# Performance work log

Hardware: AMD Instinct MI355X
Metric: run time of the kernel (lower is better)

## Reference

```python
import jax, jax.numpy as jnp
import numpy as np

N, E, F_NODE, F_EDGE = 100000, 400000, 64, 16
HID, HEADS, L, G, FP = 128, 4, 4, 1024, 2048
DH = HID // HEADS
T, K = 5, 32
EPS = 1e-5
NEG_SLOPE = 0.2


def _gat(x, src, dst, ea, Wl, bl, Wr, br, We, att, bias):
    """GATv2Conv (PyG semantics, eval mode): x_l=lin_l(x_src), x_r=lin_r(x_dst),
    e = att . leaky_relu(x_l[src] + x_r[dst] + lin_edge(edge_attr)),
    alpha = segment-softmax over dst, out = scatter-sum(alpha * x_l[src]) + bias."""
    n = x.shape[0]
    xl = (x @ Wl + bl).reshape(n, HEADS, DH)
    xr = (x @ Wr + br).reshape(n, HEADS, DH)
    ee = (ea @ We).reshape(-1, HEADS, DH)
    e = jax.nn.leaky_relu(xl[src] + xr[dst] + ee, NEG_SLOPE)  # [E,H,D]
    score = jnp.einsum('ehd,hd->eh', e, att)                   # [E,H]
    m = jax.ops.segment_max(score, dst, num_segments=n)        # stable softmax
    p = jnp.exp(score - m[dst])
    denom = jax.ops.segment_sum(p, dst, num_segments=n)
    alpha = p / (denom[dst] + 1e-16)
    out = jax.ops.segment_sum(alpha[:, :, None] * xl[src], dst, num_segments=n)
    return out.reshape(n, HID) + bias


def _bn_elu(h, g, b):
    # BatchNorm over the node dimension (training-mode batch stats) + ELU
    mu = h.mean(0)
    var = h.var(0)
    return jax.nn.elu((h - mu) / jnp.sqrt(var + EPS) * g + b)


def setup_inputs() -> dict:
    key = jax.random.key(0)
    ks = jax.random.split(key, 16)
    s_in = 1.0 / np.sqrt(F_NODE)
    s_h = 1.0 / np.sqrt(HID)
    s_e = 1.0 / np.sqrt(F_EDGE)
    Lh = L - 1
    return dict(
        x=jax.random.normal(ks[0], (N, F_NODE), jnp.float32),
        edge_index=jax.random.randint(ks[1], (2, E), 0, N),
        edge_attr=jax.random.normal(ks[2], (E, F_EDGE), jnp.float32),
        batch=jnp.sort(jax.random.randint(ks[3], (N,), 0, G)),
        morgan_fp=(jax.random.uniform(ks[4], (G, FP)) < 0.1).astype(jnp.float32),
        fp_idx=jnp.arange(T * K).reshape(T, K),
        Wl0=jax.random.normal(ks[5], (F_NODE, HID)) * s_in,
        bl0=jnp.zeros((HID,)),
        Wr0=jax.random.normal(ks[6], (F_NODE, HID)) * s_in,
        br0=jnp.zeros((HID,)),
        We0=jax.random.normal(ks[7], (F_EDGE, HID)) * s_e,
        att0=jax.random.normal(ks[8], (HEADS, DH)) * s_h,
        bias0=jnp.zeros((HID,)),
        g0=jnp.ones((HID,)),
        b0=jnp.zeros((HID,)),
        Wl=jax.random.normal(ks[9], (Lh, HID, HID)) * s_h,
        bl=jnp.zeros((Lh, HID)),
        Wr=jax.random.normal(ks[10], (Lh, HID, HID)) * s_h,
        br=jnp.zeros((Lh, HID)),
        We=jax.random.normal(ks[11], (Lh, F_EDGE, HID)) * s_e,
        att=jax.random.normal(ks[12], (Lh, HEADS, DH)) * s_h,
        biasc=jnp.zeros((Lh, HID)),
        g=jnp.ones((Lh, HID)),
        b=jnp.zeros((Lh, HID)),
        tw1=jax.random.normal(ks[13], (T, HID + K, HID)) / np.sqrt(HID + K),
        tb1=jnp.zeros((T, HID)),
        tw2=jax.random.normal(ks[14], (T, HID, 1)) * s_h,
        tb2=jnp.zeros((T, 1)),
    )


def reference(x, edge_index, edge_attr, batch, morgan_fp, fp_idx,
              Wl0, bl0, Wr0, br0, We0, att0, bias0, g0, b0,
              Wl, bl, Wr, br, We, att, biasc, g, b,
              tw1, tb1, tw2, tb2):
    src, dst = edge_index[0], edge_index[1]
    h = _bn_elu(_gat(x, src, dst, edge_attr, Wl0, bl0, Wr0, br0, We0, att0, bias0), g0, b0)
    for i in range(L - 1):  # residual stacked GATv2 layers
        h = _bn_elu(_gat(h, src, dst, edge_attr, Wl[i], bl[i], Wr[i], br[i],
                         We[i], att[i], biasc[i]), g[i], b[i]) + h
    counts = jax.ops.segment_sum(jnp.ones((h.shape[0],), h.dtype), batch, num_segments=G)
    emb = jax.ops.segment_sum(h, batch, num_segments=G) / jnp.maximum(counts, 1.0)[:, None]
    outs = []
    for t in range(T):  # per-task heads on [graph_emb ; selected fp bits]
        fused = jnp.concatenate([emb, morgan_fp[:, fp_idx[t]]], axis=1)
        hm = jax.nn.relu(fused @ tw1[t] + tb1[t])
        outs.append(hm @ tw2[t] + tb2[t])
    return jnp.concatenate(outs, axis=1)  # [G, T]
```

## Files before the change

### kernel.cpp

```cpp
#include <hip/hip_runtime.h>
#include <hip/hip_bf16.h>

#define N_NODES 100000
#define N_EDGES 400000
#define F_NODE_ 64
#define F_EDGE_ 16
#define HID_ 128
#define N_GRAPH 1024
#define N_TASK 5

typedef unsigned short u16;
typedef __attribute__((ext_vector_type(8))) short frag8;
typedef __attribute__((ext_vector_type(4))) float f32x4;
typedef __attribute__((ext_vector_type(2))) float f32x2;

__device__ __forceinline__ float bu2f(u16 v){ return __uint_as_float(((unsigned)v) << 16); }
__device__ __forceinline__ float2 bp2f(unsigned u){
  return make_float2(__uint_as_float(u << 16), __uint_as_float(u & 0xFFFF0000u));
}
__device__ __forceinline__ f32x2 bp2v(unsigned u){
  f32x2 r; r.x = __uint_as_float(u << 16); r.y = __uint_as_float(u & 0xFFFF0000u); return r;
}
__device__ __forceinline__ u16 f2bu(float f){
  __hip_bfloat16 h = __float2bfloat16(f);
  return *(u16*)&h;
}
__device__ __forceinline__ unsigned packbf(float a, float b){
  return (unsigned)f2bu(a) | ((unsigned)f2bu(b) << 16);
}

#define CAST_BLKS ((N_NODES*F_NODE_ + 255)/256)
#define EG256 ((N_EDGES + 255)/256)
#define GOFF_BLKS ((N_GRAPH + 1 + 255)/256)
__global__ __launch_bounds__(256) void k_cast_hist(const float* __restrict__ s, u16* __restrict__ d,
                                                   const int* __restrict__ ei, int* __restrict__ counts,
                                                   const int* __restrict__ batch, int* __restrict__ goff){
  int b = blockIdx.x;
  if (b < CAST_BLKS){
    int i = b*256 + threadIdx.x;
    if (i < N_NODES*F_NODE_) d[i] = f2bu(s[i]);
  } else if (b < CAST_BLKS + EG256){
    int e = (b - CAST_BLKS)*256 + threadIdx.x;
    if (e < N_EDGES) atomicAdd(&counts[ei[N_EDGES + e]], 1);
  } else {
    int g = (b - CAST_BLKS - EG256)*256 + threadIdx.x;
    if (g <= N_GRAPH){
      int lo = 0, hi = N_NODES;
      while (lo < hi){
        int mid = (lo + hi) >> 1;
        if (batch[mid] < g) lo = mid + 1; else hi = mid;
      }
      goff[g] = lo;
    }
  }
}

struct WZ12 { const float* src[12]; u16* dst[12]; int Ks[12]; int Kd[12]; };
__global__ __launch_bounds__(256) void k_wswz_all(WZ12 p){
  const int s = blockIdx.y;
  const int Kd = p.Kd[s], Ks = p.Ks[s];
  int i = blockIdx.x*256 + threadIdx.x;
  if (i >= Kd*128) return;
  int k = i >> 7, n = i & 127;
  float v = (k < Ks) ? p.src[s][k*128 + n] : 0.f;
  int kk = k & 31, c = k >> 5;
  int quad = kk >> 3, j = kk & 7;
  int nt = n >> 4;
  int lane = quad*16 + (n & 15);
  p.dst[s][(((c*8 + nt)*64) + lane)*8 + j] = f2bu(v);
}

#define GEMM_GRID ((N_NODES + 127)/128)
#define EPROJ_GRID ((N_EDGES + 127)/128)
__global__ __launch_bounds__(256) void k_gemm_eproj(const u16* __restrict__ A,
                                                    const u16* __restrict__ Wzl,
                                                    const u16* __restrict__ Wzr,
                                                    const float* __restrict__ bl,
                                                    const float* __restrict__ br,
                                                    u16* __restrict__ Cl,
                                                    u16* Cr,
                                                    int M, int K,
                                                    const u16* __restrict__ ea16,
                                                    const u16* __restrict__ Wez,
                                                    u16* __restrict__ eproj){
  __shared__ u16 WS[128*128];
  const int t = threadIdx.x;
  const int b = blockIdx.x;
  if (b < 2*GEMM_GRID){
    const int which = (b >= GEMM_GRID);
    const int bx = which ? b - GEMM_GRID : b;
    const u16*   Wz   = which ? Wzr : Wzl;
    const float* bias = which ? br  : bl;
    u16*         C    = which ? Cr  : Cl;
    {
      const uint4* src = (const uint4*)Wz;
      uint4* dst = (uint4*)WS;
      const int n = (K*128) >> 3;
      for (int i = t; i < n; i += 256) dst[i] = src[i];
    }
    __syncthreads();
    const int w = t >> 6, l = t & 63;
    const int m = l & 15, quad = l >> 4;
    const int rowA0 = bx*128 + w*32 + m;
    const int rowA1 = rowA0 + 16;
    f32x4 acc[2][8];
    #pragma unroll
    for (int i=0;i<2;i++)
      #pragma unroll
      for (int j=0;j<8;j++) acc[i][j] = (f32x4){0.f,0.f,0.f,0.f};
    const int KC = K >> 5;
    for (int c = 0; c < KC; c++){
      frag8 a0 = {}, a1 = {};
      if (rowA0 < M) a0 = *(const frag8*)(A + (size_t)rowA0*K + c*32 + quad*8);
      if (rowA1 < M) a1 = *(const frag8*)(A + (size_t)rowA1*K + c*32 + quad*8);
      #pragma unroll
      for (int nt = 0; nt < 8; nt++){
        frag8 bfr = *(const frag8*)&WS[(((c*8 + nt)*64) + l)*8];
        acc[0][nt] = __builtin_amdgcn_mfma_f32_16x16x32_bf16(a0, bfr, acc[0][nt], 0,0,0);
        acc[1][nt] = __builtin_amdgcn_mfma_f32_16x16x32_bf16(a1, bfr, acc[1][nt], 0,0,0);
      }
    }
    float bcv[8];
    #pragma unroll
    for (int nt=0; nt<8; nt++) bcv[nt] = bias[nt*16 + m];
    __syncthreads();
    const int sXor = quad << 4;
    #pragma unroll
    for (int rt = 0; rt < 2; rt++){
      #pragma unroll
      for (int r = 0; r < 4; r++){
        const int row = w*32 + rt*16 + quad*4 + r;
        #pragma unroll
        for (int nt = 0; nt < 8; nt++){
          const int col = nt*16 + m;
          WS[row*128 + (col ^ sXor)] = f2bu(acc[rt][nt][r] + bcv[nt]);
        }
      }
    }
    __syncthreads();
    #pragma unroll
    for (int i = 0; i < 8; i++){
      const int idx = i*256 + t;
      const int row = idx >> 4, k16 = idx & 15;
      const int grp = (k16*8) ^ (((row>>2)&3)<<4);
      const int grow = bx*128 + row;
      if (grow < M)
        *(uint4*)(C + (size_t)grow*128 + k16*8) = *(const uint4*)&WS[row*128 + grp];
    }
  } else {
    const int bx = b - 2*GEMM_GRID;
    {
      const uint4* s4 = (const uint4*)Wez;
      uint4* d4 = (uint4*)WS;
      for (int i = t; i < 512; i += 256) d4[i] = s4[i];
    }
    __syncthreads();
    const int w = t >> 6, l = t & 63, m = l & 15, quad = l >> 4;
    const int row0 = bx*128 + w*32 + m;
    const int row1 = row0 + 16;
    f32x4 acc[2][8];
    #pragma unroll
    for (int i=0;i<2;i++)
      #pragma unroll
      for (int j=0;j<8;j++) acc[i][j] = (f32x4){0.f,0.f,0.f,0.f};
    frag8 a0 = {}, a1 = {};
    if (quad < 2){
      a0 = *(const frag8*)(ea16 + (size_t)row0*16 + quad*8);
      a1 = *(const frag8*)(ea16 + (size_t)row1*16 + quad*8);
    }
    #pragma unroll
    for (int nt = 0; nt < 8; nt++){
      frag8 bfr = *(const frag8*)&WS[(nt*64 + l)*8];
      acc[0][nt] = __builtin_amdgcn_mfma_f32_16x16x32_bf16(a0, bfr, acc[0][nt], 0,0,0);
      acc[1][nt] = __builtin_amdgcn_mfma_f32_16x16x32_bf16(a1, bfr, acc[1][nt], 0,0,0);
    }
    __syncthreads();
    const int sXor = quad << 4;
    #pragma unroll
    for (int rt = 0; rt < 2; rt++){
      #pragma unroll
      for (int r = 0; r < 4; r++){
        const int row = w*32 + rt*16 + quad*4 + r;
        #pragma unroll
        for (int nt = 0; nt < 8; nt++){
          const int col = nt*16 + m;
          WS[row*128 + (col ^ sXor)] = f2bu(acc[rt][nt][r]);
        }
      }
    }
    __syncthreads();
    #pragma unroll
    for (int i = 0; i < 8; i++){
      const int idx = i*256 + t;
      const int row = idx >> 4, k16 = idx & 15;
      const int grp = (k16*8) ^ (((row>>2)&3)<<4);
      *(uint4*)(eproj + ((size_t)(bx*128 + row))*128 + k16*8) = *(const uint4*)&WS[row*128 + grp];
    }
  }
}

__global__ __launch_bounds__(512) void k_scan1(const int* __restrict__ counts,
                                               int* __restrict__ incl,
                                               int* __restrict__ bsum){
  __shared__ int s[512];
  const int t = threadIdx.x;
  int i = blockIdx.x*512 + t;
  int v = (i < N_NODES) ? counts[i] : 0;
  s[t] = v;
  __syncthreads();
  for (int off = 1; off < 512; off <<= 1){
    int x = (t >= off) ? s[t - off] : 0;
    __syncthreads();
    s[t] += x;
    __syncthreads();
  }
  if (i < N_NODES) incl[i] = s[t];
  if (t == 511) bsum[blockIdx.x] = s[511];
}

__global__ __launch_bounds__(256) void k_scan2(int* __restrict__ bsum, int nb){
  __shared__ int s[256];
  const int t = threadIdx.x;
  int v = (t < nb) ? bsum[t] : 0;
  s[t] = v;
  __syncthreads();
  for (int off = 1; off < 256; off <<= 1){
    int x = (t >= off) ? s[t - off] : 0;
    __syncthreads();
    s[t] += x;
    __syncthreads();
  }
  if (t < nb) bsum[t] = s[t] - v;
}

__global__ __launch_bounds__(512) void k_scan3(const int* __restrict__ counts,
                                               const int* __restrict__ incl,
                                               const int* __restrict__ bsum,
                                               int* __restrict__ offsets,
                                               int* __restrict__ cursor){
  int i = blockIdx.x*512 + threadIdx.x;
  if (i >= N_NODES) return;
  int o = bsum[blockIdx.x] + incl[i];
  offsets[i + 1] = o;
  cursor[i]      = o - counts[i];
  if (i == 0) offsets[0] = 0;
}

__global__ __launch_bounds__(256) void k_scatter(const int* __restrict__ ei,
                                                 int* __restrict__ cursor,
                                                 int* __restrict__ ssrc,
                                                 const float* __restrict__ ea,
                                                 u16* __restrict__ ea16){
  int e = blockIdx.x*256 + threadIdx.x;
  if (e >= N_EDGES) return;
  int dst = ei[N_EDGES + e];
  int pos = atomicAdd(&cursor[dst], 1);
  ssrc[pos] = ei[e];
  const float* s = ea + (size_t)e*F_EDGE_;
  unsigned p[8];
  #pragma unroll
  for (int k=0;k<8;k++) p[k] = packbf(s[2*k], s[2*k+1]);
  uint4* d4 = (uint4*)(ea16 + (size_t)pos*16);
  d4[0] = make_uint4(p[0],p[1],p[2],p[3]);
  d4[1] = make_uint4(p[4],p[5],p[6],p[7]);
}

#define GAT_GRID (N_NODES/16)
__global__ __launch_bounds__(256) void k_gat_ep(const u16* __restrict__ xl,
                                                unsigned* xr_aggr,
                                                const u16* __restrict__ eproj,
                                                const float* __restrict__ att,
                                                const int* __restrict__ offsets,
                                                const int* __restrict__ ssrc){
  const int t = threadIdx.x;
  const int wave = t >> 6, lane = t & 63;
  const int half = lane >> 5, l32 = lane & 31;
  const int c0 = l32*4;
  const float4 av = *(const float4*)(att + c0);

  for (int k = 0; k < 2; k++){
    const int node = blockIdx.x*16 + wave*4 + k*2 + half;
    const uint2 xru = *(const uint2*)(xr_aggr + (size_t)node*64 + l32*2);
    const f32x2 xr0 = bp2v(xru.x), xr1 = bp2v(xru.y);
    f32x2 acc0 = {0.f,0.f}, acc1 = {0.f,0.f};
    float den = 0.f;
    const int beg = offsets[node], end = offsets[node+1];
    int it = (end - beg + 3) >> 2;
    int oit = __shfl_xor(it, 32);
    const int maxit = it > oit ? it : oit;
    int i = beg;
    for (int n = 0; n < maxit; n++, i += 4){
      const int mm = end - i;
      int ib = (mm > 0) ? i : beg;
      ib = ib < N_EDGES ? ib : N_EDGES - 1;
      const int i0 = ib;
      const int i1 = (mm > 1) ? i+1 : ib;
      const int i2 = (mm > 2) ? i+2 : ib;
      const int i3 = (mm > 3) ? i+3 : ib;
      const int s0 = ssrc[i0], s1 = ssrc[i1], s2 = ssrc[i2], s3 = ssrc[i3];
      const uint2 e0 = *(const uint2*)(eproj + (size_t)i0*128 + c0);
      const uint2 e1 = *(const uint2*)(eproj + (size_t)i1*128 + c0);
      const uint2 e2 = *(const uint2*)(eproj + (size_t)i2*128 + c0);
      const uint2 e3 = *(const uint2*)(eproj + (size_t)i3*128 + c0);
      const uint2 x0 = *(const uint2*)(xl + (size_t)s0*HID_ + c0);
      const uint2 x1 = *(const uint2*)(xl + (size_t)s1*HID_ + c0);
      const uint2 x2 = *(const uint2*)(xl + (size_t)s2*HID_ + c0);
      const uint2 x3 = *(const uint2*)(xl + (size_t)s3*HID_ + c0);
      const f32x2 vl00 = bp2v(x0.x), vl01 = bp2v(x0.y);
      const f32x2 vl10 = bp2v(x1.x), vl11 = bp2v(x1.y);
      const f32x2 vl20 = bp2v(x2.x), vl21 = bp2v(x2.y);
      const f32x2 vl30 = bp2v(x3.x), vl31 = bp2v(x3.y);
      f32x2 v00 = vl00 + xr0 + bp2v(e0.x), v01 = vl01 + xr1 + bp2v(e0.y);
      f32x2 v10 = vl10 + xr0 + bp2v(e1.x), v11 = vl11 + xr1 + bp2v(e1.y);
      f32x2 v20 = vl20 + xr0 + bp2v(e2.x), v21 = vl21 + xr1 + bp2v(e2.y);
      f32x2 v30 = vl30 + xr0 + bp2v(e3.x), v31 = vl31 + xr1 + bp2v(e3.y);
      f32x2 w;
      w = v00*0.2f; v00.x = fmaxf(v00.x,w.x); v00.y = fmaxf(v00.y,w.y);
      w = v01*0.2f; v01.x = fmaxf(v01.x,w.x); v01.y = fmaxf(v01.y,w.y);
      w = v10*0.2f; v10.x = fmaxf(v10.x,w.x); v10.y = fmaxf(v10.y,w.y);
      w = v11*0.2f; v11.x = fmaxf(v11.x,w.x); v11.y = fmaxf(v11.y,w.y);
      w = v20*0.2f; v20.x = fmaxf(v20.x,w.x); v20.y = fmaxf(v20.y,w.y);
      w = v21*0.2f; v21.x = fmaxf(v21.x,w.x); v21.y = fmaxf(v21.y,w.y);
      w = v30*0.2f; v30.x = fmaxf(v30.x,w.x); v30.y = fmaxf(v30.y,w.y);
      w = v31*0.2f; v31.x = fmaxf(v31.x,w.x); v31.y = fmaxf(v31.y,w.y);
      float sc0 = v00.x*av.x + v00.y*av.y + v01.x*av.z + v01.y*av.w;
      float sc1 = v10.x*av.x + v10.y*av.y + v11.x*av.z + v11.y*av.w;
      float sc2 = v20.x*av.x + v20.y*av.y + v21.x*av.z + v21.y*av.w;
      float sc3 = v30.x*av.x + v30.y*av.y + v31.x*av.z + v31.y*av.w;
      sc0 += __shfl_xor(sc0, 1); sc1 += __shfl_xor(sc1, 1); sc2 += __shfl_xor(sc2, 1); sc3 += __shfl_xor(sc3, 1);
      sc0 += __shfl_xor(sc0, 2); sc1 += __shfl_xor(sc1, 2); sc2 += __shfl_xor(sc2, 2); sc3 += __shfl_xor(sc3, 2);
      sc0 += __shfl_xor(sc0, 4); sc1 += __shfl_xor(sc1, 4); sc2 += __shfl_xor(sc2, 4); sc3 += __shfl_xor(sc3, 4);
      const float p0 = (mm > 0) ? __expf(sc0) : 0.f;
      const float p1 = (mm > 1) ? __expf(sc1) : 0.f;
      const float p2 = (mm > 2) ? __expf(sc2) : 0.f;
      const float p3 = (mm > 3) ? __expf(sc3) : 0.f;
      acc0 += p0*vl00 + p1*vl10 + p2*vl20 + p3*vl30;
      acc1 += p0*vl01 + p1*vl11 + p2*vl21 + p3*vl31;
      den  += p0 + p1 + p2 + p3;
    }
    const float inv = 1.0f / (den + 1e-16f);
    uint2 outv;
    outv.x = packbf(acc0.x*inv, acc0.y*inv);
    outv.y = packbf(acc1.x*inv, acc1.y*inv);
    *(uint2*)(xr_aggr + (size_t)node*64 + l32*2) = outv;
  }
}

__global__ __launch_bounds__(256) void k_bn_stats(const unsigned* __restrict__ aggr_b,
                                                  float* __restrict__ stats){
  __shared__ float redS[4][128], redQ[4][128];
  const int t = threadIdx.x;
  const int p = t & 63, rg = t >> 6;
  const int c0 = p*2;
  float s0=0.f, s1=0.f, q0=0.f, q1=0.f;
  for (int r = blockIdx.x*4 + rg; r < N_NODES; r += gridDim.x*4){
    float2 v = bp2f(aggr_b[(size_t)r*64 + p]);
    s0 += v.x; s1 += v.y; q0 += v.x*v.x; q1 += v.y*v.y;
  }
  redS[rg][c0] = s0; redS[rg][c0+1] = s1;
  redQ[rg][c0] = q0; redQ[rg][c0+1] = q1;
  __syncthreads();
  if (rg == 0){
    #pragma unroll
    for (int g=1; g<4; g++){
      s0 += redS[g][c0]; s1 += redS[g][c0+1];
      q0 += redQ[g][c0]; q1 += redQ[g][c0+1];
    }
    atomicAdd(&stats[c0],     s0);
    atomicAdd(&stats[c0+1],   s1);
    atomicAdd(&stats[128+c0],   q0);
    atomicAdd(&stats[128+c0+1], q1);
  }
}

__global__ __launch_bounds__(256) void k_bn_apply(const unsigned* __restrict__ aggr_b,
                                                  const float* __restrict__ stats,
                                                  const float* __restrict__ gamma,
                                                  const float* __restrict__ beta,
                                                  u16* __restrict__ h, int residual){
  size_t i = (size_t)blockIdx.x*256 + threadIdx.x;
  if (i >= (size_t)N_NODES*16) return;
  const int c = (int)((i & 15) * 8);
  const float invn = 1.0f / (float)N_NODES;
  uint4 v4 = ((const uint4*)aggr_b)[i];
  uint4* hp = (uint4*)h + i;
  uint4 hv4 = make_uint4(0,0,0,0);
  if (residual) hv4 = *hp;
  unsigned vin[4]  = {v4.x, v4.y, v4.z, v4.w};
  unsigned hin[4]  = {hv4.x, hv4.y, hv4.z, hv4.w};
  unsigned outw[4];
  #pragma unroll
  for (int j=0;j<4;j++){
    int cc = c + j*2;
    float mu0  = stats[cc]   * invn,  mu1  = stats[cc+1]   * invn;
    float var0 = stats[128+cc]*invn - mu0*mu0;
    float var1 = stats[129+cc]*invn - mu1*mu1;
    float sc0 = rsqrtf(var0 + 1e-5f) * gamma[cc];
    float sc1 = rsqrtf(var1 + 1e-5f) * gamma[cc+1];
    float2 v = bp2f(vin[j]);
    float val0 = (v.x - mu0) * sc0 + beta[cc];
    float val1 = (v.y - mu1) * sc1 + beta[cc+1];
    val0 = val0 > 0.f ? val0 : expm1f(val0);
    val1 = val1 > 0.f ? val1 : expm1f(val1);
    if (residual){
      float2 hv = bp2f(hin[j]);
      val0 += hv.x; val1 += hv.y;
    }
    outw[j] = packbf(val0, val1);
  }
  *hp = make_uint4(outw[0], outw[1], outw[2], outw[3]);
}

__global__ __launch_bounds__(256) void k_pool_seg(const unsigned* __restrict__ h2,
                                                  const int* __restrict__ goff,
                                                  float* __restrict__ emb){
  __shared__ float redS[4][128];
  const int g = blockIdx.x, t = threadIdx.x;
  const int p = t & 63, rg = t >> 6;
  const int beg = goff[g], end = goff[g+1];
  float a0 = 0.f, a1 = 0.f;
  for (int r = beg + rg; r < end; r += 4){
    float2 v = bp2f(h2[(size_t)r*64 + p]);
    a0 += v.x; a1 += v.y;
  }
  redS[rg][p*2] = a0; redS[rg][p*2+1] = a1;
  __syncthreads();
  if (rg == 0){
    #pragma unroll
    for (int k=1;k<4;k++){ a0 += redS[k][p*2]; a1 += redS[k][p*2+1]; }
    float n = fmaxf((float)(end - beg), 1.f);
    emb[(size_t)g*HID_ + p*2]     = a0 / n;
    emb[(size_t)g*HID_ + p*2 + 1] = a1 / n;
  }
}

#define HG 8
__global__ __launch_bounds__(128) void k_heads(const float* __restrict__ emb,
                                               const float* __restrict__ mf,
                                               const int* __restrict__ fpi,
                                               const float* __restrict__ tw1,
                                               const float* __restrict__ tb1,
                                               const float* __restrict__ tw2,
                                               const float* __restrict__ tb2,
                                               float* __restrict__ out){
  const int task = blockIdx.y, g0 = blockIdx.x*HG;
  const int j = threadIdx.x;
  __shared__ float fused[HG][160];
  __shared__ float red[HG][128];
  for (int idx = j; idx < HG*160; idx += 128){
    int g = idx / 160, i = idx % 160;
    float v;
    if (i < 128) v = emb[(size_t)(g0+g)*HID_ + i];
    else         v = mf[(size_t)(g0+g)*2048 + fpi[task*32 + (i-128)]];
    fused[g][i] = v;
  }
  __syncthreads();
  const float* w1 = tw1 + (size_t)task*160*128;
  float acc[HG];
  float b1 = tb1[task*128 + j];
  #pragma unroll
  for (int g=0; g<HG; g++) acc[g] = b1;
  for (int i=0; i<160; i++){
    float wv = w1[(size_t)i*128 + j];
    #pragma unroll
    for (int g=0; g<HG; g++) acc[g] += fused[g][i] * wv;
  }
  float t2 = tw2[task*128 + j];
  #pragma unroll
  for (int g=0; g<HG; g++){
    float v = acc[g] > 0.f ? acc[g] : 0.f;
    red[g][j] = v * t2;
  }
  __syncthreads();
  int g = j >> 4, l16 = j & 15;
  float s = 0.f;
  #pragma unroll
  for (int k=0;k<8;k++) s += red[g][l16 + k*16];
  s += __shfl_xor(s, 1, 16);
  s += __shfl_xor(s, 2, 16);
  s += __shfl_xor(s, 4, 16);
  s += __shfl_xor(s, 8, 16);
  if (l16 == 0) out[(size_t)(g0+g)*N_TASK + task] = s + tb2[task];
}

extern "C" void kernel_launch(void* const* d_in, const int* in_sizes, int n_in,
                              void* d_out, int out_size, void* d_ws, size_t ws_size,
                              hipStream_t stream){
  const float* x    = (const float*)d_in[0];
  const int*   ei   = (const int*)  d_in[1];
  const float* ea   = (const float*)d_in[2];
  const int*   batch= (const int*)  d_in[3];
  const float* mf   = (const float*)d_in[4];
  const int*   fpi  = (const int*)  d_in[5];
  const float* Wl0  = (const float*)d_in[6];
  const float* bl0  = (const float*)d_in[7];
  const float* Wr0  = (const float*)d_in[8];
  const float* br0  = (const float*)d_in[9];
  const float* We0  = (const float*)d_in[10];
  const float* att0 = (const float*)d_in[11];
  const float* g0   = (const float*)d_in[13];
  const float* b0   = (const float*)d_in[14];
  const float* Wl   = (const float*)d_in[15];
  const float* bl   = (const float*)d_in[16];
  const float* Wr   = (const float*)d_in[17];
  const float* br   = (const float*)d_in[18];
  const float* We   = (const float*)d_in[19];
  const float* att  = (const float*)d_in[20];
  const float* gg   = (const float*)d_in[22];
  const float* bb   = (const float*)d_in[23];
  const float* tw1  = (const float*)d_in[24];
  const float* tb1  = (const float*)d_in[25];
  const float* tw2  = (const float*)d_in[26];
  const float* tb2  = (const float*)d_in[27];
  float* out = (float*)d_out;

  char* w = (char*)d_ws;
  auto alloc = [&](size_t bytes)->char*{ char* r = w; w += (bytes + 255) & ~(size_t)255; return r; };
  u16*   xl     = (u16*)  alloc((size_t)N_NODES*HID_*2);
  unsigned* xr_aggr = (unsigned*)alloc((size_t)N_NODES*64*4);
  u16*   h      = (u16*)  alloc((size_t)N_NODES*HID_*2);
  u16*   ea16   = (u16*)  alloc((size_t)N_EDGES*16*2);
  int*   counts = (int*)  alloc((size_t)N_NODES*4);
  float* stats4 = (float*)alloc(4*256*4);
  int*   offsets= (int*)  alloc((size_t)(N_NODES+1)*4);
  int*   cursor = (int*)  alloc((size_t)N_NODES*4);
  int*   incl   = (int*)  alloc((size_t)N_NODES*4);
  int*   bsum   = (int*)  alloc(256*4);
  int*   ssrc   = (int*)  alloc((size_t)N_EDGES*4);
  int*   goff   = (int*)  alloc((size_t)(N_GRAPH+1)*4);
  float* emb    = (float*)alloc((size_t)N_GRAPH*HID_*4);
  u16*   Wzl0   = (u16*)  alloc((size_t)F_NODE_*128*2);
  u16*   Wzr0   = (u16*)  alloc((size_t)F_NODE_*128*2);
  u16*   Wzl123 = (u16*)  alloc((size_t)3*HID_*128*2);
  u16*   Wzr123 = (u16*)  alloc((size_t)3*HID_*128*2);
  u16*   Wez4   = (u16*)  alloc((size_t)4*32*128*2);
  u16*   eproj  = (u16*)  alloc((size_t)N_EDGES*HID_*2);
  u16*   xbf    = (u16*)  alloc((size_t)N_NODES*F_NODE_*2);

  const size_t zlen = (size_t)((char*)(stats4 + 4*256) - (char*)counts);
  const int nscan = (N_NODES + 511)/512;

  {
    WZ12 p;
    p.src[0] = Wl0; p.dst[0] = Wzl0; p.Ks[0] = F_NODE_; p.Kd[0] = F_NODE_;
    p.src[1] = Wr0; p.dst[1] = Wzr0; p.Ks[1] = F_NODE_; p.Kd[1] = F_NODE_;
    for (int i=0;i<3;i++){
      p.src[2+i] = Wl + (size_t)i*HID_*HID_; p.dst[2+i] = Wzl123 + (size_t)i*HID_*128; p.Ks[2+i] = HID_; p.Kd[2+i] = HID_;
      p.src[5+i] = Wr + (size_t)i*HID_*HID_; p.dst[5+i] = Wzr123 + (size_t)i*HID_*128; p.Ks[5+i] = HID_; p.Kd[5+i] = HID_;
    }
    p.src[8] = We0; p.dst[8] = Wez4; p.Ks[8] = F_EDGE_; p.Kd[8] = 32;
    for (int i=0;i<3;i++){
      p.src[9+i] = We + (size_t)i*F_EDGE_*HID_; p.dst[9+i] = Wez4 + (size_t)(i+1)*32*128; p.Ks[9+i] = F_EDGE_; p.Kd[9+i] = 32;
    }
    hipLaunchKernelGGL(k_wswz_all, dim3((HID_*128 + 255)/256, 12), dim3(256), 0, stream, p);
  }
  hipMemsetAsync(counts, 0, zlen, stream);
  hipLaunchKernelGGL(k_cast_hist, dim3(CAST_BLKS + EG256 + GOFF_BLKS), dim3(256), 0, stream,
                     x, xbf, ei, counts, batch, goff);
  hipLaunchKernelGGL(k_scan1,  dim3(nscan), dim3(512), 0, stream, counts, incl, bsum);
  hipLaunchKernelGGL(k_scan2,  dim3(1),     dim3(256), 0, stream, bsum, nscan);
  hipLaunchKernelGGL(k_scan3,  dim3(nscan), dim3(512), 0, stream, counts, incl, bsum, offsets, cursor);
  hipLaunchKernelGGL(k_scatter,dim3(EG256), dim3(256), 0, stream, ei, cursor, ssrc, ea, ea16);

  for (int layer = 0; layer < 4; layer++){
    const float *bl_, *br_, *att_, *g_, *b_;
    const u16 *Wzl_, *Wzr_, *Ain;
    int K;
    if (layer == 0){
      bl_=bl0; br_=br0; att_=att0; g_=g0; b_=b0;
      Wzl_ = Wzl0; Wzr_ = Wzr0; Ain = xbf; K = F_NODE_;
    } else {
      int i = layer - 1;
      bl_ = bl + (size_t)i*HID_;  br_ = br + (size_t)i*HID_;
      att_= att + (size_t)i*HID_;
      g_  = gg + (size_t)i*HID_;  b_  = bb + (size_t)i*HID_;
      Wzl_ = Wzl123 + (size_t)i*HID_*128;
      Wzr_ = Wzr123 + (size_t)i*HID_*128;
      Ain = h; K = HID_;
    }
    float* stats = stats4 + layer*256;
    hipLaunchKernelGGL(k_gemm_eproj, dim3(2*GEMM_GRID + EPROJ_GRID), dim3(256), 0, stream,
                       Ain, Wzl_, Wzr_, bl_, br_, xl, (u16*)xr_aggr, N_NODES, K,
                       ea16, Wez4 + (size_t)layer*32*128, eproj);
    hipLaunchKernelGGL(k_gat_ep, dim3(GAT_GRID), dim3(256), 0, stream,
                       xl, xr_aggr, eproj, att_, offsets, ssrc);
    hipLaunchKernelGGL(k_bn_stats, dim3(512), dim3(256), 0, stream, xr_aggr, stats);
    hipLaunchKernelGGL(k_bn_apply, dim3((N_NODES*16 + 255)/256), dim3(256), 0, stream,
                       xr_aggr, stats, g_, b_, h, layer > 0 ? 1 : 0);
  }
  hipLaunchKernelGGL(k_pool_seg, dim3(N_GRAPH), dim3(256), 0, stream, (const unsigned*)h, goff, emb);
  hipLaunchKernelGGL(k_heads, dim3(N_GRAPH/HG, N_TASK), dim3(128), 0, stream, emb, mf, fpi, tw1, tb1, tw2, tb2, out);
}
```

Before: 781.9 us.

## Fuse BN statistics into GAT kernel and merge setup kernels

Batch-norm sum and sum-of-squares accumulation moves into the GAT aggregation epilogue. Each block now processes four node tiles and does one block-level reduction followed by atomics, so the separate stats pass that re-read the aggregated output is gone. The weight-swizzle kernel is folded into the cast/histogram launch, and the block-sum scan is folded into scan3, which saves several launches. In exchange the GAT grid is four times smaller and every scan3 block redundantly rescans the block sums.

```diff
diff --git a/kernel.cpp b/kernel.cpp
--- a/kernel.cpp
+++ b/kernel.cpp
@@ -29,12 +29,16 @@
   return (unsigned)f2bu(a) | ((unsigned)f2bu(b) << 16);
 }
 
+struct WZ12 { const float* src[12]; u16* dst[12]; int Ks[12]; int Kd[12]; };
+
 #define CAST_BLKS ((N_NODES*F_NODE_ + 255)/256)
 #define EG256 ((N_EDGES + 255)/256)
 #define GOFF_BLKS ((N_GRAPH + 1 + 255)/256)
+#define WSWZ_BLKS (12*64)
 __global__ __launch_bounds__(256) void k_cast_hist(const float* __restrict__ s, u16* __restrict__ d,
                                                    const int* __restrict__ ei, int* __restrict__ counts,
-                                                   const int* __restrict__ batch, int* __restrict__ goff){
+                                                   const int* __restrict__ batch, int* __restrict__ goff,
+                                                   WZ12 p){
   int b = blockIdx.x;
   if (b < CAST_BLKS){
     int i = b*256 + threadIdx.x;
@@ -42,7 +46,7 @@
   } else if (b < CAST_BLKS + EG256){
     int e = (b - CAST_BLKS)*256 + threadIdx.x;
     if (e < N_EDGES) atomicAdd(&counts[ei[N_EDGES + e]], 1);
-  } else {
+  } else if (b < CAST_BLKS + EG256 + GOFF_BLKS){
     int g = (b - CAST_BLKS - EG256)*256 + threadIdx.x;
     if (g <= N_GRAPH){
       int lo = 0, hi = N_NODES;
@@ -52,22 +56,20 @@
       }
       goff[g] = lo;
     }
-  }
-}
-
-struct WZ12 { const float* src[12]; u16* dst[12]; int Ks[12]; int Kd[12]; };
-__global__ __launch_bounds__(256) void k_wswz_all(WZ12 p){
-  const int s = blockIdx.y;
-  const int Kd = p.Kd[s], Ks = p.Ks[s];
-  int i = blockIdx.x*256 + threadIdx.x;
-  if (i >= Kd*128) return;
-  int k = i >> 7, n = i & 127;
-  float v = (k < Ks) ? p.src[s][k*128 + n] : 0.f;
-  int kk = k & 31, c = k >> 5;
-  int quad = kk >> 3, j = kk & 7;
-  int nt = n >> 4;
-  int lane = quad*16 + (n & 15);
-  p.dst[s][(((c*8 + nt)*64) + lane)*8 + j] = f2bu(v);
+  } else {
+    int bb = b - CAST_BLKS - EG256 - GOFF_BLKS;
+    const int sW = bb >> 6;
+    const int Kd = p.Kd[sW], Ks = p.Ks[sW];
+    int i = (bb & 63)*256 + threadIdx.x;
+    if (i >= Kd*128) return;
+    int k = i >> 7, n = i & 127;
+    float v = (k < Ks) ? p.src[sW][k*128 + n] : 0.f;
+    int kk = k & 31, c = k >> 5;
+    int quad = kk >> 3, j = kk & 7;
+    int nt = n >> 4;
+    int lane = quad*16 + (n & 15);
+    p.dst[sW][(((c*8 + nt)*64) + lane)*8 + j] = f2bu(v);
+  }
 }
 
 #define GEMM_GRID ((N_NODES + 127)/128)
@@ -218,29 +220,26 @@
   if (t == 511) bsum[blockIdx.x] = s[511];
 }
 
-__global__ __launch_bounds__(256) void k_scan2(int* __restrict__ bsum, int nb){
-  __shared__ int s[256];
+__global__ __launch_bounds__(512) void k_scan3(const int* __restrict__ counts,
+                                               const int* __restrict__ incl,
+                                               const int* __restrict__ bsum, int nb,
+                                               int* __restrict__ offsets,
+                                               int* __restrict__ cursor){
+  __shared__ int sb[256];
   const int t = threadIdx.x;
-  int v = (t < nb) ? bsum[t] : 0;
-  s[t] = v;
+  if (t < 256) sb[t] = (t < nb) ? bsum[t] : 0;
   __syncthreads();
   for (int off = 1; off < 256; off <<= 1){
-    int x = (t >= off) ? s[t - off] : 0;
-    __syncthreads();
-    s[t] += x;
-    __syncthreads();
-  }
-  if (t < nb) bsum[t] = s[t] - v;
-}
-
-__global__ __launch_bounds__(512) void k_scan3(const int* __restrict__ counts,
-                                               const int* __restrict__ incl,
-                                               const int* __restrict__ bsum,
-                                               int* __restrict__ offsets,
-                                               int* __restrict__ cursor){
-  int i = blockIdx.x*512 + threadIdx.x;
+    int x = 0;
+    if (t < 256 && t >= off) x = sb[t - off];
+    __syncthreads();
+    if (t < 256) sb[t] += x;
+    __syncthreads();
+  }
+  int i = blockIdx.x*512 + t;
   if (i >= N_NODES) return;
-  int o = bsum[blockIdx.x] + incl[i];
+  int pre = (blockIdx.x == 0) ? 0 : sb[blockIdx.x - 1];
+  int o = pre + incl[i];
   offsets[i + 1] = o;
   cursor[i]      = o - counts[i];
   if (i == 0) offsets[0] = 0;
@@ -265,111 +264,106 @@
   d4[1] = make_uint4(p[4],p[5],p[6],p[7]);
 }
 
-#define GAT_GRID (N_NODES/16)
+#define GAT_TILES (N_NODES/16)
+#define GAT_BLOCKS ((GAT_TILES + 3)/4)
 __global__ __launch_bounds__(256) void k_gat_ep(const u16* __restrict__ xl,
                                                 unsigned* xr_aggr,
                                                 const u16* __restrict__ eproj,
                                                 const float* __restrict__ att,
                                                 const int* __restrict__ offsets,
-                                                const int* __restrict__ ssrc){
+                                                const int* __restrict__ ssrc,
+                                                float* __restrict__ stats){
+  __shared__ float red[8][264];
   const int t = threadIdx.x;
   const int wave = t >> 6, lane = t & 63;
   const int half = lane >> 5, l32 = lane & 31;
   const int c0 = l32*4;
   const float4 av = *(const float4*)(att + c0);
-
-  for (int k = 0; k < 2; k++){
-    const int node = blockIdx.x*16 + wave*4 + k*2 + half;
-    const uint2 xru = *(const uint2*)(xr_aggr + (size_t)node*64 + l32*2);
-    const f32x2 xr0 = bp2v(xru.x), xr1 = bp2v(xru.y);
-    f32x2 acc0 = {0.f,0.f}, acc1 = {0.f,0.f};
-    float den = 0.f;
-    const int beg = offsets[node], end = offsets[node+1];
-    int it = (end - beg + 3) >> 2;
-    int oit = __shfl_xor(it, 32);
-    const int maxit = it > oit ? it : oit;
-    int i = beg;
-    for (int n = 0; n < maxit; n++, i += 4){
-      const int mm = end - i;
-      int ib = (mm > 0) ? i : beg;
-      ib = ib < N_EDGES ? ib : N_EDGES - 1;
-      const int i0 = ib;
-      const int i1 = (mm > 1) ? i+1 : ib;
-      const int i2 = (mm > 2) ? i+2 : ib;
-      const int i3 = (mm > 3) ? i+3 : ib;
-      const int s0 = ssrc[i0], s1 = ssrc[i1], s2 = ssrc[i2], s3 = ssrc[i3];
-      const uint2 e0 = *(const uint2*)(eproj + (size_t)i0*128 + c0);
-      const uint2 e1 = *(const uint2*)(eproj + (size_t)i1*128 + c0);
-      const uint2 e2 = *(const uint2*)(eproj + (size_t)i2*128 + c0);
-      const uint2 e3 = *(const uint2*)(eproj + (size_t)i3*128 + c0);
-      const uint2 x0 = *(const uint2*)(xl + (size_t)s0*HID_ + c0);
-      const uint2 x1 = *(const uint2*)(xl + (size_t)s1*HID_ + c0);
-      const uint2 x2 = *(const uint2*)(xl + (size_t)s2*HID_ + c0);
-      const uint2 x3 = *(const uint2*)(xl + (size_t)s3*HID_ + c0);
-      const f32x2 vl00 = bp2v(x0.x), vl01 = bp2v(x0.y);
-      const f32x2 vl10 = bp2v(x1.x), vl11 = bp2v(x1.y);
-      const f32x2 vl20 = bp2v(x2.x), vl21 = bp2v(x2.y);
-      const f32x2 vl30 = bp2v(x3.x), vl31 = bp2v(x3.y);
-      f32x2 v00 = vl00 + xr0 + bp2v(e0.x), v01 = vl01 + xr1 + bp2v(e0.y);
-      f32x2 v10 = vl10 + xr0 + bp2v(e1.x), v11 = vl11 + xr1 + bp2v(e1.y);
-      f32x2 v20 = vl20 + xr0 + bp2v(e2.x), v21 = vl21 + xr1 + bp2v(e2.y);
-      f32x2 v30 = vl30 + xr0 + bp2v(e3.x), v31 = vl31 + xr1 + bp2v(e3.y);
-      f32x2 w;
-      w = v00*0.2f; v00.x = fmaxf(v00.x,w.x); v00.y = fmaxf(v00.y,w.y);
-      w = v01*0.2f; v01.x = fmaxf(v01.x,w.x); v01.y = fmaxf(v01.y,w.y);
-      w = v10*0.2f; v10.x = fmaxf(v10.x,w.x); v10.y = fmaxf(v10.y,w.y);
-      w = v11*0.2f; v11.x = fmaxf(v11.x,w.x); v11.y = fmaxf(v11.y,w.y);
-      w = v20*0.2f; v20.x = fmaxf(v20.x,w.x); v20.y = fmaxf(v20.y,w.y);
-      w = v21*0.2f; v21.x = fmaxf(v21.x,w.x); v21.y = fmaxf(v21.y,w.y);
-      w = v30*0.2f; v30.x = fmaxf(v30.x,w.x); v30.y = fmaxf(v30.y,w.y);
-      w = v31*0.2f; v31.x = fmaxf(v31.x,w.x); v31.y = fmaxf(v31.y,w.y);
-      float sc0 = v00.x*av.x + v00.y*av.y + v01.x*av.z + v01.y*av.w;
-      float sc1 = v10.x*av.x + v10.y*av.y + v11.x*av.z + v11.y*av.w;
-      float sc2 = v20.x*av.x + v20.y*av.y + v21.x*av.z + v21.y*av.w;
-      float sc3 = v30.x*av.x + v30.y*av.y + v31.x*av.z + v31.y*av.w;
-      sc0 += __shfl_xor(sc0, 1); sc1 += __shfl_xor(sc1, 1); sc2 += __shfl_xor(sc2, 1); sc3 += __shfl_xor(sc3, 1);
-      sc0 += __shfl_xor(sc0, 2); sc1 += __shfl_xor(sc1, 2); sc2 += __shfl_xor(sc2, 2); sc3 += __shfl_xor(sc3, 2);
-      sc0 += __shfl_xor(sc0, 4); sc1 += __shfl_xor(sc1, 4); sc2 += __shfl_xor(sc2, 4); sc3 += __shfl_xor(sc3, 4);
-      const float p0 = (mm > 0) ? __expf(sc0) : 0.f;
-      const float p1 = (mm > 1) ? __expf(sc1) : 0.f;
-      const float p2 = (mm > 2) ? __expf(sc2) : 0.f;
-      const float p3 = (mm > 3) ? __expf(sc3) : 0.f;
-      acc0 += p0*vl00 + p1*vl10 + p2*vl20 + p3*vl30;
-      acc1 += p0*vl01 + p1*vl11 + p2*vl21 + p3*vl31;
-      den  += p0 + p1 + p2 + p3;
-    }
-    const float inv = 1.0f / (den + 1e-16f);
-    uint2 outv;
-    outv.x = packbf(acc0.x*inv, acc0.y*inv);
-    outv.y = packbf(acc1.x*inv, acc1.y*inv);
-    *(uint2*)(xr_aggr + (size_t)node*64 + l32*2) = outv;
-  }
-}
-
-__global__ __launch_bounds__(256) void k_bn_stats(const unsigned* __restrict__ aggr_b,
-                                                  float* __restrict__ stats){
-  __shared__ float redS[4][128], redQ[4][128];
-  const int t = threadIdx.x;
-  const int p = t & 63, rg = t >> 6;
-  const int c0 = p*2;
-  float s0=0.f, s1=0.f, q0=0.f, q1=0.f;
-  for (int r = blockIdx.x*4 + rg; r < N_NODES; r += gridDim.x*4){
-    float2 v = bp2f(aggr_b[(size_t)r*64 + p]);
-    s0 += v.x; s1 += v.y; q0 += v.x*v.x; q1 += v.y*v.y;
-  }
-  redS[rg][c0] = s0; redS[rg][c0+1] = s1;
-  redQ[rg][c0] = q0; redQ[rg][c0+1] = q1;
+  float ss0=0.f, ss1=0.f, ss2=0.f, ss3=0.f;
+  float qq0=0.f, qq1=0.f, qq2=0.f, qq3=0.f;
+
+  for (int j = 0; j < 4; j++){
+    const int tile = blockIdx.x*4 + j;
+    if (tile >= GAT_TILES) break;
+    for (int k = 0; k < 2; k++){
+      const int node = tile*16 + wave*4 + k*2 + half;
+      const uint2 xru = *(const uint2*)(xr_aggr + (size_t)node*64 + l32*2);
+      const f32x2 xr0 = bp2v(xru.x), xr1 = bp2v(xru.y);
+      f32x2 acc0 = {0.f,0.f}, acc1 = {0.f,0.f};
+      float den = 0.f;
+      const int beg = offsets[node], end = offsets[node+1];
+      int it = (end - beg + 3) >> 2;
+      int oit = __shfl_xor(it, 32);
+      const int maxit = it > oit ? it : oit;
+      int i = beg;
+      for (int n = 0; n < maxit; n++, i += 4){
+        const int mm = end - i;
+        int ib = (mm > 0) ? i : beg;
+        ib = ib < N_EDGES ? ib : N_EDGES - 1;
+        const int i0 = ib;
+        const int i1 = (mm > 1) ? i+1 : ib;
+        const int i2 = (mm > 2) ? i+2 : ib;
+        const int i3 = (mm > 3) ? i+3 : ib;
+        const int s0 = ssrc[i0], s1 = ssrc[i1], s2 = ssrc[i2], s3 = ssrc[i3];
+        const uint2 e0 = *(const uint2*)(eproj + (size_t)i0*128 + c0);
+        const uint2 e1 = *(const uint2*)(eproj + (size_t)i1*128 + c0);
+        const uint2 e2 = *(const uint2*)(eproj + (size_t)i2*128 + c0);
+        const uint2 e3 = *(const uint2*)(eproj + (size_t)i3*128 + c0);
+        const uint2 x0 = *(const uint2*)(xl + (size_t)s0*HID_ + c0);
+        const uint2 x1 = *(const uint2*)(xl + (size_t)s1*HID_ + c0);
+        const uint2 x2 = *(const uint2*)(xl + (size_t)s2*HID_ + c0);
+        const uint2 x3 = *(const uint2*)(xl + (size_t)s3*HID_ + c0);
+        const f32x2 vl00 = bp2v(x0.x), vl01 = bp2v(x0.y);
+        const f32x2 vl10 = bp2v(x1.x), vl11 = bp2v(x1.y);
+        const f32x2 vl20 = bp2v(x2.x), vl21 = bp2v(x2.y);
+        const f32x2 vl30 = bp2v(x3.x), vl31 = bp2v(x3.y);
+        f32x2 v00 = vl00 + xr0 + bp2v(e0.x), v01 = vl01 + xr1 + bp2v(e0.y);
+        f32x2 v10 = vl10 + xr0 + bp2v(e1.x), v11 = vl11 + xr1 + bp2v(e1.y);
+        f32x2 v20 = vl20 + xr0 + bp2v(e2.x), v21 = vl21 + xr1 + bp2v(e2.y);
+        f32x2 v30 = vl30 + xr0 + bp2v(e3.x), v31 = vl31 + xr1 + bp2v(e3.y);
+        f32x2 w;
+        w = v00*0.2f; v00.x = fmaxf(v00.x,w.x); v00.y = fmaxf(v00.y,w.y);
+        w = v01*0.2f; v01.x = fmaxf(v01.x,w.x); v01.y = fmaxf(v01.y,w.y);
+        w = v10*0.2f; v10.x = fmaxf(v10.x,w.x); v10.y = fmaxf(v10.y,w.y);
+        w = v11*0.2f; v11.x = fmaxf(v11.x,w.x); v11.y = fmaxf(v11.y,w.y);
+        w = v20*0.2f; v20.x = fmaxf(v20.x,w.x); v20.y = fmaxf(v20.y,w.y);
+        w = v21*0.2f; v21.x = fmaxf(v21.x,w.x); v21.y = fmaxf(v21.y,w.y);
+        w = v30*0.2f; v30.x = fmaxf(v30.x,w.x); v30.y = fmaxf(v30.y,w.y);
+        w = v31*0.2f; v31.x = fmaxf(v31.x,w.x); v31.y = fmaxf(v31.y,w.y);
+        float sc0 = v00.x*av.x + v00.y*av.y + v01.x*av.z + v01.y*av.w;
+        float sc1 = v10.x*av.x + v10.y*av.y + v11.x*av.z + v11.y*av.w;
+        float sc2 = v20.x*av.x + v20.y*av.y + v21.x*av.z + v21.y*av.w;
+        float sc3 = v30.x*av.x + v30.y*av.y + v31.x*av.z + v31.y*av.w;
+        sc0 += __shfl_xor(sc0, 1); sc1 += __shfl_xor(sc1, 1); sc2 += __shfl_xor(sc2, 1); sc3 += __shfl_xor(sc3, 1);
+        sc0 += __shfl_xor(sc0, 2); sc1 += __shfl_xor(sc1, 2); sc2 += __shfl_xor(sc2, 2); sc3 += __shfl_xor(sc3, 2);
+        sc0 += __shfl_xor(sc0, 4); sc1 += __shfl_xor(sc1, 4); sc2 += __shfl_xor(sc2, 4); sc3 += __shfl_xor(sc3, 4);
+        const float p0 = (mm > 0) ? __expf(sc0) : 0.f;
+        const float p1 = (mm > 1) ? __expf(sc1) : 0.f;
+        const float p2 = (mm > 2) ? __expf(sc2) : 0.f;
+        const float p3 = (mm > 3) ? __expf(sc3) : 0.f;
+        acc0 += p0*vl00 + p1*vl10 + p2*vl20 + p3*vl30;
+        acc1 += p0*vl01 + p1*vl11 + p2*vl21 + p3*vl31;
+        den  += p0 + p1 + p2 + p3;
+      }
+      const float inv = 1.0f / (den + 1e-16f);
+      uint2 outv;
+      outv.x = packbf(acc0.x*inv, acc0.y*inv);
+      outv.y = packbf(acc1.x*inv, acc1.y*inv);
+      *(uint2*)(xr_aggr + (size_t)node*64 + l32*2) = outv;
+      const float2 o0 = bp2f(outv.x), o1 = bp2f(outv.y);
+      ss0 += o0.x; ss1 += o0.y; ss2 += o1.x; ss3 += o1.y;
+      qq0 += o0.x*o0.x; qq1 += o0.y*o0.y; qq2 += o1.x*o1.x; qq3 += o1.y*o1.y;
+    }
+  }
+  const int g = wave*2 + half;
+  red[g][c0+0] = ss0; red[g][c0+1] = ss1; red[g][c0+2] = ss2; red[g][c0+3] = ss3;
+  red[g][128+c0+0] = qq0; red[g][128+c0+1] = qq1; red[g][128+c0+2] = qq2; red[g][128+c0+3] = qq3;
   __syncthreads();
-  if (rg == 0){
-    #pragma unroll
-    for (int g=1; g<4; g++){
-      s0 += redS[g][c0]; s1 += redS[g][c0+1];
-      q0 += redQ[g][c0]; q1 += redQ[g][c0+1];
-    }
-    atomicAdd(&stats[c0],     s0);
-    atomicAdd(&stats[c0+1],   s1);
-    atomicAdd(&stats[128+c0],   q0);
-    atomicAdd(&stats[128+c0+1], q1);
+  {
+    float a = 0.f;
+    #pragma unroll
+    for (int gg = 0; gg < 8; gg++) a += red[gg][t];
+    atomicAdd(&stats[t], a);
   }
 }
 
@@ -540,26 +534,23 @@
   const size_t zlen = (size_t)((char*)(stats4 + 4*256) - (char*)counts);
   const int nscan = (N_NODES + 511)/512;
 
-  {
-    WZ12 p;
-    p.src[0] = Wl0; p.dst[0] = Wzl0; p.Ks[0] = F_NODE_; p.Kd[0] = F_NODE_;
-    p.src[1] = Wr0; p.dst[1] = Wzr0; p.Ks[1] = F_NODE_; p.Kd[1] = F_NODE_;
-    for (int i=0;i<3;i++){
-      p.src[2+i] = Wl + (size_t)i*HID_*HID_; p.dst[2+i] = Wzl123 + (size_t)i*HID_*128; p.Ks[2+i] = HID_; p.Kd[2+i] = HID_;
-      p.src[5+i] = Wr + (size_t)i*HID_*HID_; p.dst[5+i] = Wzr123 + (size_t)i*HID_*128; p.Ks[5+i] = HID_; p.Kd[5+i] = HID_;
-    }
-    p.src[8] = We0; p.dst[8] = Wez4; p.Ks[8] = F_EDGE_; p.Kd[8] = 32;
-    for (int i=0;i<3;i++){
-      p.src[9+i] = We + (size_t)i*F_EDGE_*HID_; p.dst[9+i] = Wez4 + (size_t)(i+1)*32*128; p.Ks[9+i] = F_EDGE_; p.Kd[9+i] = 32;
-    }
-    hipLaunchKernelGGL(k_wswz_all, dim3((HID_*128 + 255)/256, 12), dim3(256), 0, stream, p);
-  }
+  WZ12 p;
+  p.src[0] = Wl0; p.dst[0] = Wzl0; p.Ks[0] = F_NODE_; p.Kd[0] = F_NODE_;
+  p.src[1] = Wr0; p.dst[1] = Wzr0; p.Ks[1] = F_NODE_; p.Kd[1] = F_NODE_;
+  for (int i=0;i<3;i++){
+    p.src[2+i] = Wl + (size_t)i*HID_*HID_; p.dst[2+i] = Wzl123 + (size_t)i*HID_*128; p.Ks[2+i] = HID_; p.Kd[2+i] = HID_;
+    p.src[5+i] = Wr + (size_t)i*HID_*HID_; p.dst[5+i] = Wzr123 + (size_t)i*HID_*128; p.Ks[5+i] = HID_; p.Kd[5+i] = HID_;
+  }
+  p.src[8] = We0; p.dst[8] = Wez4; p.Ks[8] = F_EDGE_; p.Kd[8] = 32;
+  for (int i=0;i<3;i++){
+    p.src[9+i] = We + (size_t)i*F_EDGE_*HID_; p.dst[9+i] = Wez4 + (size_t)(i+1)*32*128; p.Ks[9+i] = F_EDGE_; p.Kd[9+i] = 32;
+  }
+
   hipMemsetAsync(counts, 0, zlen, stream);
-  hipLaunchKernelGGL(k_cast_hist, dim3(CAST_BLKS + EG256 + GOFF_BLKS), dim3(256), 0, stream,
-                     x, xbf, ei, counts, batch, goff);
+  hipLaunchKernelGGL(k_cast_hist, dim3(CAST_BLKS + EG256 + GOFF_BLKS + WSWZ_BLKS), dim3(256), 0, stream,
+                     x, xbf, ei, counts, batch, goff, p);
   hipLaunchKernelGGL(k_scan1,  dim3(nscan), dim3(512), 0, stream, counts, incl, bsum);
-  hipLaunchKernelGGL(k_scan2,  dim3(1),     dim3(256), 0, stream, bsum, nscan);
-  hipLaunchKernelGGL(k_scan3,  dim3(nscan), dim3(512), 0, stream, counts, incl, bsum, offsets, cursor);
+  hipLaunchKernelGGL(k_scan3,  dim3(nscan), dim3(512), 0, stream, counts, incl, bsum, nscan, offsets, cursor);
   hipLaunchKernelGGL(k_scatter,dim3(EG256), dim3(256), 0, stream, ei, cursor, ssrc, ea, ea16);
 
   for (int layer = 0; layer < 4; layer++){
@@ -582,9 +573,8 @@
     hipLaunchKernelGGL(k_gemm_eproj, dim3(2*GEMM_GRID + EPROJ_GRID), dim3(256), 0, stream,
                        Ain, Wzl_, Wzr_, bl_, br_, xl, (u16*)xr_aggr, N_NODES, K,
                        ea16, Wez4 + (size_t)layer*32*128, eproj);
-    hipLaunchKernelGGL(k_gat_ep, dim3(GAT_GRID), dim3(256), 0, stream,
-                       xl, xr_aggr, eproj, att_, offsets, ssrc);
-    hipLaunchKernelGGL(k_bn_stats, dim3(512), dim3(256), 0, stream, xr_aggr, stats);
+    hipLaunchKernelGGL(k_gat_ep, dim3(GAT_BLOCKS), dim3(256), 0, stream,
+                       xl, xr_aggr, eproj, att_, offsets, ssrc, stats);
     hipLaunchKernelGGL(k_bn_apply, dim3((N_NODES*16 + 255)/256), dim3(256), 0, stream,
                        xr_aggr, stats, g_, b_, h, layer > 0 ? 1 : 0);
   }
```

Measured after the change: 761.6 us. 2.6% less time.
